# Optimization experiments

Measured on AMD Instinct MI355X. Metric: run time of the kernel, lower is better.

## Reference

```python
import jax, jax.numpy as jnp
import numpy as np

C_IN = 256
C_QK = C_IN // 8   # 32
C_V = C_IN // 2    # 128


def conv3x3(x, w):
    # x: [B, Cin, H, W], w: [Cout, Cin, 3, 3]; stride 1, padding 1 == SAME
    return jax.lax.conv_general_dilated(
        x, w, window_strides=(1, 1), padding='SAME',
        dimension_numbers=('NCHW', 'OIHW', 'NCHW'))


def setup_inputs() -> dict:
    key = jax.random.key(0)
    ks = jax.random.split(key, 6)
    B, V, T = 16, 64, 64
    x = jax.random.normal(ks[0], (B, C_IN, V, T), dtype=jnp.float32)
    wq = jax.random.normal(ks[1], (C_QK, C_IN, 3, 3), dtype=jnp.float32) * 0.02
    wk = jax.random.normal(ks[2], (C_QK, C_IN, 3, 3), dtype=jnp.float32) * 0.02
    wv = jax.random.normal(ks[3], (C_V, C_IN, 3, 3), dtype=jnp.float32) * 0.02
    wo = jax.random.normal(ks[4], (C_IN, C_V, 3, 3), dtype=jnp.float32) * 0.02
    sigma = jnp.full((1,), 0.5, dtype=jnp.float32)  # nn.Parameter(torch.zeros(1)) init; nonzero for testing
    return {'x': x, 'wq': wq, 'wk': wk, 'wv': wv, 'wo': wo, 'sigma': sigma}


def reference(x, wq, wk, wv, wo, sigma):
    # x: [B, C, V, T]
    q = conv3x3(x, wq).transpose(0, 3, 2, 1)  # [B, T, V, Cqk]
    k = conv3x3(x, wk).transpose(0, 3, 2, 1)  # [B, T, V, Cqk]
    v = conv3x3(x, wv).transpose(0, 3, 2, 1)  # [B, T, V, Cv]
    # attention over the V axis, independently per (B, T)
    attn = jax.nn.softmax(jnp.einsum('btvc,btwc->btvw', q, k), axis=-1)  # [B,T,V,V]
    av = jnp.einsum('btvw,btwc->btvc', attn, v)  # [B, T, V, Cv]
    av = av.transpose(0, 3, 2, 1)                # [B, Cv, V, T]
    out = x + sigma * conv3x3(av, wo)            # [B, C, V, T]
    B, T, V, _ = attn.shape
    return out, attn.reshape(B * T, V, V)
```

## Files before the change

kernel.cpp:

```cpp
#include <hip/hip_runtime.h>
#include <hip/hip_bf16.h>

typedef __hip_bfloat16 bf16;
typedef float f32x4 __attribute__((ext_vector_type(4)));
typedef short s16x8 __attribute__((ext_vector_type(8)));

#define B_   16
#define CIN  256
#define CQK  32
#define CV   128
#define VDIM 64
#define TDIM 64
#define P    (VDIM * TDIM)

static __device__ __forceinline__ ushort f2bf(float f) {
    bf16 h = __float2bfloat16(f);
    return *(ushort*)&h;
}
static __device__ __forceinline__ float bf2f(ushort u) {
    bf16 h = *(bf16*)&u;
    return __bfloat162float(h);
}

static __device__ __forceinline__ void gld16(const void* gsrc, void* ldst) {
    __builtin_amdgcn_global_load_lds(
        (const __attribute__((address_space(1))) void*)gsrc,
        (__attribute__((address_space(3))) void*)ldst,
        16, 0, 0);
}

#define MFMA16(A, B, C) __builtin_amdgcn_mfma_f32_16x16x32_bf16((A), (B), (C), 0, 0, 0)

__global__ __launch_bounds__(256) void repack_all(
    const float* __restrict__ x,
    const float* __restrict__ wq, const float* __restrict__ wk,
    const float* __restrict__ wv, const float* __restrict__ wo,
    ushort* __restrict__ xhd,
    ushort* __restrict__ wvT, ushort* __restrict__ woT,
    ushort* __restrict__ wqh,
    ushort* __restrict__ zp)
{
    if (blockIdx.x >= 1024) {
        if (blockIdx.x == 1024) ((uint*)zp)[threadIdx.x] = 0;
        int i = (blockIdx.x - 1024) * 256 + threadIdx.x;
        const int NQK = 9 * 64 * 256;
        const int NV  = 9 * 128 * 256;
        if (i < NQK) {
            int tap = i / (64 * 256);
            int r   = i % (64 * 256);
            int oc  = r >> 8;
            int ci  = r & 255;
            const float* src = (oc < 32) ? wq : wk;
            wqh[i] = f2bf(src[(size_t)(oc & 31) * 2304 + ci * 9 + tap]);
        } else if (i < NQK + NV) {
            i -= NQK;
            int tap = i / (128 * 256);
            int r   = i % (128 * 256);
            int oc  = r >> 8;
            int ci  = r & 255;
            wvT[i] = f2bf(wv[(size_t)oc * 2304 + ci * 9 + tap]);
        } else {
            i -= NQK + NV;
            int tap = i / (256 * 128);
            int r   = i % (256 * 128);
            int oc  = r >> 7;
            int ci  = r & 127;
            woT[i] = f2bf(wo[(size_t)oc * 1152 + ci * 9 + tap]);
        }
        return;
    }
    const int b = blockIdx.x >> 6;
    const int y = blockIdx.x & 63;
    __shared__ ushort th[64][257];
    const int t  = threadIdx.x & 63;
    const int cq = threadIdx.x >> 6;
    const float* xb = x + (((size_t)b * CIN) * VDIM + y) * TDIM;
    for (int ci = cq; ci < 256; ci += 4)
        th[t][ci] = f2bf(xb[(size_t)ci * P + t]);
    __syncthreads();
    const int ci4 = (threadIdx.x & 63) * 4;
    const int tr0 = threadIdx.x >> 6;
    for (int tr = tr0; tr < 64; tr += 4) {
        ushort4 uh;
        uh.x = th[tr][ci4];     uh.y = th[tr][ci4 + 1];
        uh.z = th[tr][ci4 + 2]; uh.w = th[tr][ci4 + 3];
        *(ushort4*)(xhd + ((((size_t)b * 64 + tr) * 64 + y) * 256 + ci4)) = uh;
    }
}

#define STAGE2(SRC, CI0)                                                          \
    {                                                                             \
        const int i0 = (w < 2) ? w * 17 : 34 + (w - 2) * 16;                      \
        const int nr = (w < 2) ? 17 : 16;                                         \
        for (int j = 0; j < nr; ++j) {                                            \
            const int ii  = i0 + j;                                               \
            const int row = ii * 4 + (lane >> 4);                                 \
            const int dxs = (row * 993) >> 16;                                    \
            const int yl  = row - dxs * 66;                                       \
            const int tp  = t0 + dxs - 1;                                         \
            const int yp  = yl - 1;                                               \
            const int chg = (lane & 15) ^ (row & 7);                              \
            const bool ok = ((unsigned)tp < 64u) && ((unsigned)yp < 64u);         \
            const ushort* sp = ok                                                 \
                ? (SRC) + ((((size_t)b * 64 + tp) * 64 + yp) * 256 + (CI0) + chg * 8) \
                : zp + (size_t)lane * 8;                                          \
            gld16(sp, btile + ii * 1024);                                         \
        }                                                                         \
    }

#define READ_BFR(BFR, DY, DXS, KK)                                                \
    {                                                                             \
        _Pragma("unroll")                                                         \
        for (int nf = 0; nf < 4; ++nf) {                                          \
            const int ylr = nf * 16 + (lane & 15) + (DY);                         \
            const int row = (DXS) * 66 + ylr;                                     \
            BFR[nf] = *(const s16x8*)(btile + row * 256 +                         \
                       ((((KK) * 64 + (lane >> 4) * 16)) ^ ((row & 7) << 4)));    \
        }                                                                         \
    }

__global__ __launch_bounds__(256) void qkvattn2(
    const ushort* __restrict__ xh,
    const ushort* __restrict__ wvT,
    const ushort* __restrict__ wqh,
    const ushort* __restrict__ zp,
    float* __restrict__ attn_out, ushort* __restrict__ av)
{
    const int bid  = ((blockIdx.x & 7) << 6) | (blockIdx.x >> 3);
    const int b    = bid >> 5;
    const int t0   = (bid & 31) * 2;
    const int tid  = threadIdx.x;
    const int lane = tid & 63;
    const int w    = tid >> 6;

    __shared__ __align__(16) char smem[67584];
    char* btile = smem;

    f32x4 accv[2][2][4];
    f32x4 accq[2][4];
#pragma unroll
    for (int c = 0; c < 2; ++c) {
#pragma unroll
        for (int m = 0; m < 2; ++m)
#pragma unroll
            for (int nf = 0; nf < 4; ++nf) accv[c][m][nf] = (f32x4){0.f, 0.f, 0.f, 0.f};
#pragma unroll
        for (int nf = 0; nf < 4; ++nf) accq[c][nf] = (f32x4){0.f, 0.f, 0.f, 0.f};
    }

    const int ocv  = w * 32 + (lane & 15);
    const int ocqk = w * 16 + (lane & 15);
    const int ko8  = (lane >> 4) * 8;

#define WVO(TAP, M, KK) (const s16x8*)(wvT + (size_t)((TAP) * 128 + ocv + (M) * 16) * 256 + ci0 + (KK) * 32 + ko8)
#define WQO(TAP, KK) (const s16x8*)(wqh + (size_t)((TAP) * 64 + ocqk) * 256 + ci0 + (KK) * 32 + ko8)

    for (int chunk = 0; chunk < 2; ++chunk) {
        const int ci0 = chunk * 128;

        __syncthreads();
        STAGE2(xh, ci0)
        __syncthreads();

#pragma unroll 1
        for (int tap = 0; tap < 9; ++tap) {
            const int dy = tap / 3, dxp = tap % 3;
            s16x8 va[4], vb[4], ha[4];
#pragma unroll
            for (int kk = 0; kk < 4; ++kk) {
                va[kk] = *WVO(tap, 0, kk);
                vb[kk] = *WVO(tap, 1, kk);
                ha[kk] = *WQO(tap, kk);
            }
#pragma unroll
            for (int kk = 0; kk < 4; ++kk) {
                s16x8 bfr[4];
                READ_BFR(bfr, dy, dxp, kk)
#pragma unroll
                for (int nf = 0; nf < 4; ++nf)
                    accv[0][0][nf] = MFMA16(va[kk], bfr[nf], accv[0][0][nf]);
#pragma unroll
                for (int nf = 0; nf < 4; ++nf)
                    accv[0][1][nf] = MFMA16(vb[kk], bfr[nf], accv[0][1][nf]);
#pragma unroll
                for (int nf = 0; nf < 4; ++nf)
                    accq[0][nf] = MFMA16(ha[kk], bfr[nf], accq[0][nf]);

                s16x8 bfr1[4];
                READ_BFR(bfr1, dy, dxp + 1, kk)
#pragma unroll
                for (int nf = 0; nf < 4; ++nf)
                    accv[1][0][nf] = MFMA16(va[kk], bfr1[nf], accv[1][0][nf]);
#pragma unroll
                for (int nf = 0; nf < 4; ++nf)
                    accv[1][1][nf] = MFMA16(vb[kk], bfr1[nf], accv[1][1][nf]);
#pragma unroll
                for (int nf = 0; nf < 4; ++nf)
                    accq[1][nf] = MFMA16(ha[kk], bfr1[nf], accq[1][nf]);
            }
        }
    }
#undef WVO
#undef WQO
    __syncthreads();

    const int l15 = lane & 15, lg = lane >> 4;

#pragma unroll
    for (int col = 0; col < 2; ++col) {
        {
            char* qkb = smem + ((w < 2) ? 0 : 8192);
            const int c0 = (w & 1) * 16 + lg * 4;
#pragma unroll
            for (int nf = 0; nf < 4; ++nf) {
                const int y = nf * 16 + l15;
                ushort4 h4, l4;
#pragma unroll
                for (int r = 0; r < 4; ++r) {
                    ushort h = f2bf(accq[col][nf][r]);
                    ((ushort*)&h4)[r] = h;
                    ((ushort*)&l4)[r] = f2bf(accq[col][nf][r] - bf2f(h));
                }
                const int swz = (y & 7) << 4;
                *(ushort4*)(qkb + y * 128 + ((2 * c0) ^ swz))      = h4;
                *(ushort4*)(qkb + y * 128 + ((64 + 2 * c0) ^ swz)) = l4;
            }
#pragma unroll
            for (int m = 0; m < 2; ++m)
#pragma unroll
                for (int nf = 0; nf < 4; ++nf) {
                    const int y = nf * 16 + l15;
#pragma unroll
                    for (int r = 0; r < 4; ++r) {
                        const int oc = w * 32 + m * 16 + lg * 4 + r;
                        *(ushort*)(smem + 16384 + oc * 128 + ((2 * y) ^ ((oc & 7) << 4)))
                            = f2bf(accv[col][m][nf][r]);
                    }
                }
        }
        __syncthreads();

        f32x4 pv[4];
        {
            const int yq = w * 16 + l15;
            const int sq = (yq & 7) << 4;
            s16x8 qh = *(const s16x8*)(smem + yq * 128 + ((lg * 16) ^ sq));
            s16x8 ql = *(const s16x8*)(smem + yq * 128 + ((64 + lg * 16) ^ sq));
            s16x8 kh[4], kl[4];
#pragma unroll
            for (int jt = 0; jt < 4; ++jt) {
                const int jr = jt * 16 + l15;
                const int sk = (jr & 7) << 4;
                kh[jt] = *(const s16x8*)(smem + 8192 + jr * 128 + ((lg * 16) ^ sk));
                kl[jt] = *(const s16x8*)(smem + 8192 + jr * 128 + ((64 + lg * 16) ^ sk));
            }
            __syncthreads();

            f32x4 sAcc[4];
#pragma unroll
            for (int jt = 0; jt < 4; ++jt) {
                f32x4 a = (f32x4){0.f, 0.f, 0.f, 0.f};
                a = MFMA16(qh, kh[jt], a);
                a = MFMA16(qh, kl[jt], a);
                a = MFMA16(ql, kh[jt], a);
                sAcc[jt] = a;
            }
            float mx[4], sum[4];
#pragma unroll
            for (int r = 0; r < 4; ++r)
                mx[r] = fmaxf(fmaxf(sAcc[0][r], sAcc[1][r]), fmaxf(sAcc[2][r], sAcc[3][r]));
#pragma unroll
            for (int d = 1; d < 16; d <<= 1)
#pragma unroll
                for (int r = 0; r < 4; ++r) mx[r] = fmaxf(mx[r], __shfl_xor(mx[r], d));
#pragma unroll
            for (int r = 0; r < 4; ++r) sum[r] = 0.f;
#pragma unroll
            for (int jt = 0; jt < 4; ++jt)
#pragma unroll
                for (int r = 0; r < 4; ++r) {
                    pv[jt][r] = expf(sAcc[jt][r] - mx[r]);
                    sum[r] += pv[jt][r];
                }
#pragma unroll
            for (int d = 1; d < 16; d <<= 1)
#pragma unroll
                for (int r = 0; r < 4; ++r) sum[r] += __shfl_xor(sum[r], d);
#pragma unroll
            for (int r = 0; r < 4; ++r) sum[r] = 1.f / sum[r];
#pragma unroll
            for (int jt = 0; jt < 4; ++jt)
#pragma unroll
                for (int r = 0; r < 4; ++r) pv[jt][r] *= sum[r];

            float* ao = attn_out + (size_t)(b * 64 + t0 + col) * 4096;
#pragma unroll
            for (int jt = 0; jt < 4; ++jt)
#pragma unroll
                for (int r = 0; r < 4; ++r)
                    ao[(w * 16 + lg * 4 + r) * 64 + jt * 16 + l15] = pv[jt][r];

#pragma unroll
            for (int jt = 0; jt < 4; ++jt)
#pragma unroll
                for (int r = 0; r < 4; ++r) {
                    const int i = w * 16 + lg * 4 + r;
                    const int j = jt * 16 + l15;
                    const int off = i * 128 + ((2 * j) ^ ((i & 7) << 4));
                    ushort h = f2bf(pv[jt][r]);
                    *(ushort*)(smem + off)        = h;
                    *(ushort*)(smem + 8192 + off) = f2bf(pv[jt][r] - bf2f(h));
                }
        }
        __syncthreads();

        {
            s16x8 vt[2][2];
#pragma unroll
            for (int c2 = 0; c2 < 2; ++c2)
#pragma unroll
                for (int ks = 0; ks < 2; ++ks) {
                    const int c = (w * 2 + c2) * 16 + l15;
                    vt[c2][ks] = *(const s16x8*)(smem + 16384 + c * 128 +
                                                 ((ks * 64 + lg * 16) ^ ((c & 7) << 4)));
                }
            __syncthreads();

            f32x4 acc2[2][4];
#pragma unroll
            for (int c2 = 0; c2 < 2; ++c2)
#pragma unroll
                for (int it = 0; it < 4; ++it) acc2[c2][it] = (f32x4){0.f, 0.f, 0.f, 0.f};

#pragma unroll
            for (int it = 0; it < 4; ++it) {
                const int i = it * 16 + l15;
                const int si = (i & 7) << 4;
                s16x8 ph[2], pl[2];
#pragma unroll
                for (int ks = 0; ks < 2; ++ks) {
                    ph[ks] = *(const s16x8*)(smem + i * 128 + ((ks * 64 + lg * 16) ^ si));
                    pl[ks] = *(const s16x8*)(smem + 8192 + i * 128 + ((ks * 64 + lg * 16) ^ si));
                }
#pragma unroll
                for (int c2 = 0; c2 < 2; ++c2)
#pragma unroll
                    for (int ks = 0; ks < 2; ++ks) {
                        acc2[c2][it] = MFMA16(vt[c2][ks], ph[ks], acc2[c2][it]);
                        acc2[c2][it] = MFMA16(vt[c2][ks], pl[ks], acc2[c2][it]);
                    }
            }
#pragma unroll
            for (int c2 = 0; c2 < 2; ++c2)
#pragma unroll
                for (int it = 0; it < 4; ++it)
#pragma unroll
                    for (int r = 0; r < 4; ++r) {
                        const int c = (w * 2 + c2) * 16 + lg * 4 + r;
                        const int i = it * 16 + l15;
                        *(ushort*)(smem + 16384 + i * 256 + ((2 * c) ^ ((i & 7) << 4)))
                            = f2bf(acc2[c2][it][r]);
                    }
        }
        __syncthreads();

        {
            uint* avg = (uint*)(av + (size_t)(b * 64 + t0 + col) * 8192);
#pragma unroll
            for (int t = 0; t < 16; ++t) {
                const int idx = t * 256 + tid;
                const int i  = idx >> 6;
                const int cc = idx & 63;
                avg[idx] = *(const uint*)(smem + 16384 + i * 256 + ((4 * cc) ^ ((i & 7) << 4)));
            }
        }
        __syncthreads();
    }
}

__global__ __launch_bounds__(512) void out_conv_mfma2(
    const float* __restrict__ x,
    const ushort* __restrict__ av,
    const ushort* __restrict__ woT,
    const ushort* __restrict__ zp,
    const float* __restrict__ sigma,
    float* __restrict__ out)
{
    const int bid  = ((blockIdx.x & 7) << 6) | (blockIdx.x >> 3);
    const int y0   = (bid & 31) * 2;
    const int b    = bid >> 5;
    const int tid  = threadIdx.x;
    const int lane = tid & 63;
    const int w    = tid >> 6;

    __shared__ __align__(16) char smem[67584];
    char* btile = smem;

    f32x4 acc[2][2][4];
#pragma unroll
    for (int c = 0; c < 2; ++c)
#pragma unroll
        for (int m = 0; m < 2; ++m)
#pragma unroll
            for (int nf = 0; nf < 4; ++nf) acc[c][m][nf] = (f32x4){0.f, 0.f, 0.f, 0.f};

    {
        const int i0 = (w < 2) ? w * 9 : 18 + (w - 2) * 8;
        const int ni = (w < 2) ? 9 : 8;
        for (int j = 0; j < ni; ++j) {
            const int ii  = i0 + j;
            const int row = ii * 4 + (lane >> 4);
            const int dys = (row * 993) >> 16;
            const int tl  = row - dys * 66;
            const int yp  = y0 + dys - 1;
            const int tp  = tl - 1;
            const int chg = (lane & 15) ^ (row & 7);
            const bool ok = ((unsigned)yp < 64u) && ((unsigned)tp < 64u);
            const ushort* sp = ok
                ? av + ((((size_t)b * 64 + tp) * 64 + yp) * 128 + chg * 8)
                : zp + (size_t)lane * 8;
            gld16(sp, btile + ii * 1024);
        }
    }
    __syncthreads();

    const int oc  = w * 32 + (lane & 15);
    const int ko8 = (lane >> 4) * 8;
#define WOO(TAP, M, KK) (const s16x8*)(woT + (size_t)((TAP) * 256 + oc + (M) * 16) * 128 + (KK) * 32 + ko8)
#pragma unroll 1
    for (int tap = 0; tap < 9; ++tap) {
        const int dy = tap / 3, dxp = tap % 3;
        s16x8 wa[4], wb[4];
#pragma unroll
        for (int kk = 0; kk < 4; ++kk) {
            wa[kk] = *WOO(tap, 0, kk);
            wb[kk] = *WOO(tap, 1, kk);
        }
#pragma unroll
        for (int kk = 0; kk < 4; ++kk) {
#pragma unroll
            for (int col = 0; col < 2; ++col) {
                s16x8 bfr[4];
#pragma unroll
                for (int nf = 0; nf < 4; ++nf) {
                    const int tl = nf * 16 + (lane & 15) + dxp;
                    const int row = (dy + col) * 66 + tl;
                    const int bir = kk * 64 + (lane >> 4) * 16;
                    bfr[nf] = *(const s16x8*)(btile + row * 256 + (bir ^ ((row & 7) << 4)));
                }
#pragma unroll
                for (int nf = 0; nf < 4; ++nf)
                    acc[col][0][nf] = MFMA16(wa[kk], bfr[nf], acc[col][0][nf]);
#pragma unroll
                for (int nf = 0; nf < 4; ++nf)
                    acc[col][1][nf] = MFMA16(wb[kk], bfr[nf], acc[col][1][nf]);
            }
        }
    }
#undef WOO

    const float s = sigma[0];
#pragma unroll
    for (int col = 0; col < 2; ++col)
#pragma unroll
        for (int m = 0; m < 2; ++m)
#pragma unroll
            for (int nf = 0; nf < 4; ++nf)
#pragma unroll
                for (int r = 0; r < 4; ++r) {
                    const int occ = w * 32 + m * 16 + (lane >> 4) * 4 + r;
                    const int t   = nf * 16 + (lane & 15);
                    const size_t a = (((size_t)b * 256 + occ) * 64 + (y0 + col)) * 64 + t;
                    out[a] = x[a] + s * acc[col][m][nf][r];
                }
}

extern "C" void kernel_launch(void* const* d_in, const int* in_sizes, int n_in,
                              void* d_out, int out_size, void* d_ws, size_t ws_size,
                              hipStream_t stream)
{
    const float* x     = (const float*)d_in[0];
    const float* wq    = (const float*)d_in[1];
    const float* wk    = (const float*)d_in[2];
    const float* wv    = (const float*)d_in[3];
    const float* wo    = (const float*)d_in[4];
    const float* sigma = (const float*)d_in[5];

    float* out      = (float*)d_out;
    float* attn_out = out + (size_t)16777216;

    ushort* xh = (ushort*)d_out;

    ushort* av  = (ushort*)d_ws;
    ushort* wvT = av + 8388608;
    ushort* woT = wvT + 294912;
    ushort* wqh = woT + 294912;
    ushort* zp  = wqh + 147456;

    repack_all<<<1024 + 2880, 256, 0, stream>>>(x, wq, wk, wv, wo,
                                                xh, wvT, woT, wqh, zp);
    qkvattn2<<<B_ * 32, 256, 0, stream>>>(xh, wvT, wqh, zp, attn_out, av);
    out_conv_mfma2<<<B_ * 32, 512, 0, stream>>>(x, av, woT, zp, sigma, out);
}
```

Baseline: 150.9 us.

## Process both attention columns concurrently with per-column shared-memory regions

The attention epilogue used to handle the two time columns one after another, with all four waves on each column and several barriers per column. It now stages Q/K/V for both columns into separate shared-memory regions up front. Each pair of waves then owns one column and does twice the rows and channels, which roughly halves the number of block-wide barriers. The costs are more shared memory (two regions of about 33 KB each), more registers per wave (larger vt and acc2 arrays), and possibly lower occupancy. The AV output store is also vectorised to ushort4.

```diff
diff --git a/kernel.cpp b/kernel.cpp
--- a/kernel.cpp
+++ b/kernel.cpp
@@ -205,64 +205,73 @@
     __syncthreads();
 
     const int l15 = lane & 15, lg = lane >> 4;
+    const int colw = w >> 1;
+    const int w2   = w & 1;
+    char* ovl = smem + colw * 33792;
 
 #pragma unroll
     for (int col = 0; col < 2; ++col) {
-        {
-            char* qkb = smem + ((w < 2) ? 0 : 8192);
-            const int c0 = (w & 1) * 16 + lg * 4;
+        char* o   = smem + col * 33792;
+        char* qkb = o + ((w < 2) ? 0 : 8192);
+        const int c0 = (w & 1) * 16 + lg * 4;
+#pragma unroll
+        for (int nf = 0; nf < 4; ++nf) {
+            const int y = nf * 16 + l15;
+            ushort4 h4, l4;
+#pragma unroll
+            for (int r = 0; r < 4; ++r) {
+                ushort h = f2bf(accq[col][nf][r]);
+                ((ushort*)&h4)[r] = h;
+                ((ushort*)&l4)[r] = f2bf(accq[col][nf][r] - bf2f(h));
+            }
+            const int swz = (y & 7) << 4;
+            *(ushort4*)(qkb + y * 128 + ((2 * c0) ^ swz))      = h4;
+            *(ushort4*)(qkb + y * 128 + ((64 + 2 * c0) ^ swz)) = l4;
+        }
+#pragma unroll
+        for (int m = 0; m < 2; ++m)
 #pragma unroll
             for (int nf = 0; nf < 4; ++nf) {
                 const int y = nf * 16 + l15;
-                ushort4 h4, l4;
 #pragma unroll
                 for (int r = 0; r < 4; ++r) {
-                    ushort h = f2bf(accq[col][nf][r]);
-                    ((ushort*)&h4)[r] = h;
-                    ((ushort*)&l4)[r] = f2bf(accq[col][nf][r] - bf2f(h));
+                    const int oc = w * 32 + m * 16 + lg * 4 + r;
+                    *(ushort*)(o + 16384 + oc * 128 + ((2 * y) ^ ((oc & 7) << 4)))
+                        = f2bf(accv[col][m][nf][r]);
                 }
-                const int swz = (y & 7) << 4;
-                *(ushort4*)(qkb + y * 128 + ((2 * c0) ^ swz))      = h4;
-                *(ushort4*)(qkb + y * 128 + ((64 + 2 * c0) ^ swz)) = l4;
-            }
-#pragma unroll
-            for (int m = 0; m < 2; ++m)
-#pragma unroll
-                for (int nf = 0; nf < 4; ++nf) {
-                    const int y = nf * 16 + l15;
-#pragma unroll
-                    for (int r = 0; r < 4; ++r) {
-                        const int oc = w * 32 + m * 16 + lg * 4 + r;
-                        *(ushort*)(smem + 16384 + oc * 128 + ((2 * y) ^ ((oc & 7) << 4)))
-                            = f2bf(accv[col][m][nf][r]);
-                    }
-                }
+            }
+    }
+    __syncthreads();
+
+    {
+        s16x8 kh[4], kl[4];
+#pragma unroll
+        for (int jt = 0; jt < 4; ++jt) {
+            const int jr = jt * 16 + l15;
+            const int sk = (jr & 7) << 4;
+            kh[jt] = *(const s16x8*)(ovl + 8192 + jr * 128 + ((lg * 16) ^ sk));
+            kl[jt] = *(const s16x8*)(ovl + 8192 + jr * 128 + ((64 + lg * 16) ^ sk));
+        }
+        s16x8 qh[2], ql[2];
+#pragma unroll
+        for (int s = 0; s < 2; ++s) {
+            const int yq = (w2 * 2 + s) * 16 + l15;
+            const int sq = (yq & 7) << 4;
+            qh[s] = *(const s16x8*)(ovl + yq * 128 + ((lg * 16) ^ sq));
+            ql[s] = *(const s16x8*)(ovl + yq * 128 + ((64 + lg * 16) ^ sq));
         }
         __syncthreads();
 
-        f32x4 pv[4];
-        {
-            const int yq = w * 16 + l15;
-            const int sq = (yq & 7) << 4;
-            s16x8 qh = *(const s16x8*)(smem + yq * 128 + ((lg * 16) ^ sq));
-            s16x8 ql = *(const s16x8*)(smem + yq * 128 + ((64 + lg * 16) ^ sq));
-            s16x8 kh[4], kl[4];
-#pragma unroll
-            for (int jt = 0; jt < 4; ++jt) {
-                const int jr = jt * 16 + l15;
-                const int sk = (jr & 7) << 4;
-                kh[jt] = *(const s16x8*)(smem + 8192 + jr * 128 + ((lg * 16) ^ sk));
-                kl[jt] = *(const s16x8*)(smem + 8192 + jr * 128 + ((64 + lg * 16) ^ sk));
-            }
-            __syncthreads();
-
+        float* ao = attn_out + (size_t)(b * 64 + t0 + colw) * 4096;
+#pragma unroll
+        for (int s = 0; s < 2; ++s) {
             f32x4 sAcc[4];
 #pragma unroll
             for (int jt = 0; jt < 4; ++jt) {
                 f32x4 a = (f32x4){0.f, 0.f, 0.f, 0.f};
-                a = MFMA16(qh, kh[jt], a);
-                a = MFMA16(qh, kl[jt], a);
-                a = MFMA16(ql, kh[jt], a);
+                a = MFMA16(qh[s], kh[jt], a);
+                a = MFMA16(qh[s], kl[jt], a);
+                a = MFMA16(ql[s], kh[jt], a);
                 sAcc[jt] = a;
             }
             float mx[4], sum[4];
@@ -275,6 +284,7 @@
                 for (int r = 0; r < 4; ++r) mx[r] = fmaxf(mx[r], __shfl_xor(mx[r], d));
 #pragma unroll
             for (int r = 0; r < 4; ++r) sum[r] = 0.f;
+            f32x4 pv[4];
 #pragma unroll
             for (int jt = 0; jt < 4; ++jt)
 #pragma unroll
@@ -293,88 +303,87 @@
 #pragma unroll
                 for (int r = 0; r < 4; ++r) pv[jt][r] *= sum[r];
 
-            float* ao = attn_out + (size_t)(b * 64 + t0 + col) * 4096;
 #pragma unroll
             for (int jt = 0; jt < 4; ++jt)
 #pragma unroll
                 for (int r = 0; r < 4; ++r)
-                    ao[(w * 16 + lg * 4 + r) * 64 + jt * 16 + l15] = pv[jt][r];
+                    ao[((w2 * 2 + s) * 16 + lg * 4 + r) * 64 + jt * 16 + l15] = pv[jt][r];
 
 #pragma unroll
             for (int jt = 0; jt < 4; ++jt)
 #pragma unroll
                 for (int r = 0; r < 4; ++r) {
-                    const int i = w * 16 + lg * 4 + r;
+                    const int i = (w2 * 2 + s) * 16 + lg * 4 + r;
                     const int j = jt * 16 + l15;
                     const int off = i * 128 + ((2 * j) ^ ((i & 7) << 4));
                     ushort h = f2bf(pv[jt][r]);
-                    *(ushort*)(smem + off)        = h;
-                    *(ushort*)(smem + 8192 + off) = f2bf(pv[jt][r] - bf2f(h));
+                    *(ushort*)(ovl + off)        = h;
+                    *(ushort*)(ovl + 8192 + off) = f2bf(pv[jt][r] - bf2f(h));
                 }
         }
+    }
+    __syncthreads();
+
+    {
+        s16x8 vt[4][2];
+#pragma unroll
+        for (int c2 = 0; c2 < 4; ++c2)
+#pragma unroll
+            for (int ks = 0; ks < 2; ++ks) {
+                const int c = (w2 * 4 + c2) * 16 + l15;
+                vt[c2][ks] = *(const s16x8*)(ovl + 16384 + c * 128 +
+                                             ((ks * 64 + lg * 16) ^ ((c & 7) << 4)));
+            }
         __syncthreads();
 
-        {
-            s16x8 vt[2][2];
-#pragma unroll
-            for (int c2 = 0; c2 < 2; ++c2)
+        f32x4 acc2[4][4];
+#pragma unroll
+        for (int c2 = 0; c2 < 4; ++c2)
+#pragma unroll
+            for (int it = 0; it < 4; ++it) acc2[c2][it] = (f32x4){0.f, 0.f, 0.f, 0.f};
+
+#pragma unroll
+        for (int it = 0; it < 4; ++it) {
+            const int i = it * 16 + l15;
+            const int si = (i & 7) << 4;
+            s16x8 ph[2], pl[2];
+#pragma unroll
+            for (int ks = 0; ks < 2; ++ks) {
+                ph[ks] = *(const s16x8*)(ovl + i * 128 + ((ks * 64 + lg * 16) ^ si));
+                pl[ks] = *(const s16x8*)(ovl + 8192 + i * 128 + ((ks * 64 + lg * 16) ^ si));
+            }
+#pragma unroll
+            for (int c2 = 0; c2 < 4; ++c2)
 #pragma unroll
                 for (int ks = 0; ks < 2; ++ks) {
-                    const int c = (w * 2 + c2) * 16 + l15;
-                    vt[c2][ks] = *(const s16x8*)(smem + 16384 + c * 128 +
-                                                 ((ks * 64 + lg * 16) ^ ((c & 7) << 4)));
+                    acc2[c2][it] = MFMA16(vt[c2][ks], ph[ks], acc2[c2][it]);
+                    acc2[c2][it] = MFMA16(vt[c2][ks], pl[ks], acc2[c2][it]);
                 }
-            __syncthreads();
-
-            f32x4 acc2[2][4];
-#pragma unroll
-            for (int c2 = 0; c2 < 2; ++c2)
-#pragma unroll
-                for (int it = 0; it < 4; ++it) acc2[c2][it] = (f32x4){0.f, 0.f, 0.f, 0.f};
-
+        }
+#pragma unroll
+        for (int c2 = 0; c2 < 4; ++c2)
 #pragma unroll
             for (int it = 0; it < 4; ++it) {
-                const int i = it * 16 + l15;
-                const int si = (i & 7) << 4;
-                s16x8 ph[2], pl[2];
-#pragma unroll
-                for (int ks = 0; ks < 2; ++ks) {
-                    ph[ks] = *(const s16x8*)(smem + i * 128 + ((ks * 64 + lg * 16) ^ si));
-                    pl[ks] = *(const s16x8*)(smem + 8192 + i * 128 + ((ks * 64 + lg * 16) ^ si));
-                }
-#pragma unroll
-                for (int c2 = 0; c2 < 2; ++c2)
-#pragma unroll
-                    for (int ks = 0; ks < 2; ++ks) {
-                        acc2[c2][it] = MFMA16(vt[c2][ks], ph[ks], acc2[c2][it]);
-                        acc2[c2][it] = MFMA16(vt[c2][ks], pl[ks], acc2[c2][it]);
-                    }
-            }
-#pragma unroll
-            for (int c2 = 0; c2 < 2; ++c2)
-#pragma unroll
-                for (int it = 0; it < 4; ++it)
-#pragma unroll
-                    for (int r = 0; r < 4; ++r) {
-                        const int c = (w * 2 + c2) * 16 + lg * 4 + r;
-                        const int i = it * 16 + l15;
-                        *(ushort*)(smem + 16384 + i * 256 + ((2 * c) ^ ((i & 7) << 4)))
-                            = f2bf(acc2[c2][it][r]);
-                    }
-        }
-        __syncthreads();
-
-        {
-            uint* avg = (uint*)(av + (size_t)(b * 64 + t0 + col) * 8192);
-#pragma unroll
-            for (int t = 0; t < 16; ++t) {
-                const int idx = t * 256 + tid;
-                const int i  = idx >> 6;
-                const int cc = idx & 63;
-                avg[idx] = *(const uint*)(smem + 16384 + i * 256 + ((4 * cc) ^ ((i & 7) << 4)));
-            }
-        }
-        __syncthreads();
+                const int c0 = (w2 * 4 + c2) * 16 + lg * 4;
+                const int i  = it * 16 + l15;
+                ushort4 u4;
+#pragma unroll
+                for (int r = 0; r < 4; ++r) ((ushort*)&u4)[r] = f2bf(acc2[c2][it][r]);
+                *(ushort4*)(ovl + 16384 + i * 256 + ((2 * c0) ^ ((i & 7) << 4))) = u4;
+            }
+    }
+    __syncthreads();
+
+    {
+        const int tc = tid & 127;
+        uint* avg = (uint*)(av + (size_t)(b * 64 + t0 + colw) * 8192);
+#pragma unroll
+        for (int t = 0; t < 32; ++t) {
+            const int idx = t * 128 + tc;
+            const int i  = idx >> 6;
+            const int cc = idx & 63;
+            avg[idx] = *(const uint*)(ovl + 16384 + i * 256 + ((4 * cc) ^ ((i & 7) << 4)));
+        }
     }
 }
 
```

Result: faster. 146.9 us (-2.7%).
